# Kernel optimization log

Measured on AMD Instinct MI355X. Metric: run time of the kernel, lower is better.

## Reference

```python
import jax, jax.numpy as jnp
import numpy as np

FS, R, ULAW = 160, 2, 256  # frame_size, n_samples_per_step, 2**ulaw


def _conv1d(x, w, b):
    # x: [B,C,L], w: [O,I,3], VALID conv (PyTorch Conv1d, no padding)
    y = jax.lax.conv_general_dilated(x, w, (1,), 'VALID',
                                     dimension_numbers=('NCH', 'OIH', 'NCH'))
    return y + b[None, :, None]


def _gru(x, Wih, Whh, bih, bhh):
    # PyTorch GRU (batch_first), gate order r,z,n. x: [B,T,In] -> [B,T,H]
    B = x.shape[0]
    H = Whh.shape[1]
    xW = jnp.einsum('bti,gi->btg', x, Wih) + bih  # precompute input gates [B,T,3H]
    def step(h, xw):
        gh = h @ Whh.T + bhh
        r = jax.nn.sigmoid(xw[:, :H] + gh[:, :H])
        z = jax.nn.sigmoid(xw[:, H:2 * H] + gh[:, H:2 * H])
        n = jnp.tanh(xw[:, 2 * H:] + r * gh[:, 2 * H:])
        h = (1.0 - z) * n + z * h
        return h, h
    h0 = jnp.zeros((B, H), x.dtype)
    _, ys = jax.lax.scan(step, h0, jnp.swapaxes(xW, 0, 1))
    return jnp.swapaxes(ys, 0, 1)


def _mdense(x, w1, w2, b1, b2, f1, f2):
    return jnp.tanh(x @ w1.T + b1) * f1 + jnp.tanh(x @ w2.T + b2) * f2


def setup_inputs() -> dict:
    key = jax.random.key(0)
    ks = jax.random.split(key, 40)
    B, NF, NBF = 64, 15, 20
    T = (NF - 4) * FS  # 1760: two VALID k=3 convs -> 11 frames
    EP, ES, DF, H1, H2 = 64, 128, 128, 384, 16
    IN_A = 3 * ES * R + DF   # 896
    IN_B = H1 + DF           # 512
    p = lambda k, shape, s=0.1: (s * jax.random.normal(k, shape)).astype(jnp.float32)
    d = {
        'in_data': jax.random.randint(ks[0], (B, T, 3), 0, ULAW),
        'features': jax.random.normal(ks[1], (B, NF, NBF), jnp.float32),
        'periods': jax.random.randint(ks[2], (B, NF, 1), 0, 256),
        'targets': jax.random.randint(ks[3], (B, T), 0, ULAW),
        'embed_pitch': p(ks[4], (256, EP)),
        'embed_sig': p(ks[5], (ULAW, ES)),
        'conv1_w': p(ks[6], (DF, EP + NBF, 3)), 'conv1_b': p(ks[7], (DF,)),
        'conv2_w': p(ks[8], (DF, DF, 3)), 'conv2_b': p(ks[9], (DF,)),
        'fd1_w': p(ks[10], (DF, DF)), 'fd1_b': p(ks[11], (DF,)),
        'fd2_w': p(ks[12], (DF, DF)), 'fd2_b': p(ks[13], (DF,)),
        'ga_wih': p(ks[14], (3 * H1, IN_A)), 'ga_whh': p(ks[15], (3 * H1, H1)),
        'ga_bih': p(ks[16], (3 * H1,)), 'ga_bhh': p(ks[17], (3 * H1,)),
        'gb_wih': p(ks[18], (3 * H2, IN_B)), 'gb_whh': p(ks[19], (3 * H2, H2)),
        'gb_bih': p(ks[20], (3 * H2,)), 'gb_bhh': p(ks[21], (3 * H2,)),
        'md1_w1': p(ks[22], (ULAW, H2)), 'md1_w2': p(ks[23], (ULAW, H2)),
        'md1_b1': p(ks[24], (ULAW,)), 'md1_b2': p(ks[25], (ULAW,)),
        'md1_f1': jnp.ones((ULAW,), jnp.float32), 'md1_f2': jnp.ones((ULAW,), jnp.float32),
        'md2_w1': p(ks[26], (ULAW, H2 + ES)), 'md2_w2': p(ks[27], (ULAW, H2 + ES)),
        'md2_b1': p(ks[28], (ULAW,)), 'md2_b2': p(ks[29], (ULAW,)),
        'md2_f1': jnp.ones((ULAW,), jnp.float32), 'md2_f2': jnp.ones((ULAW,), jnp.float32),
    }
    return d


def reference(in_data, features, periods, targets, embed_pitch, embed_sig,
              conv1_w, conv1_b, conv2_w, conv2_b, fd1_w, fd1_b, fd2_w, fd2_b,
              ga_wih, ga_whh, ga_bih, ga_bhh, gb_wih, gb_whh, gb_bih, gb_bhh,
              md1_w1, md1_w2, md1_b1, md1_b2, md1_f1, md1_f2,
              md2_w1, md2_w2, md2_b1, md2_b2, md2_f1, md2_f2):
    B, T = targets.shape
    # frame-rate feature network
    pitch = embed_pitch[periods[..., 0]]                  # [B,15,EP]
    cat = jnp.concatenate([features, pitch], axis=-1)      # [B,15,NBF+EP]
    x = jnp.swapaxes(cat, 1, 2)                            # [B,C,15]
    x = jnp.tanh(_conv1d(x, conv1_w, conv1_b))
    x = jnp.tanh(_conv1d(x, conv2_w, conv2_b))             # [B,DF,11]
    f = jnp.swapaxes(x, 1, 2)
    f = jnp.tanh(f @ fd1_w.T + fd1_b)
    f = jnp.tanh(f @ fd2_w.T + fd2_b)                      # [B,11,DF]
    rep = jnp.repeat(f, FS // R, axis=1)                   # [B,880,DF]
    # sample-rate network (bunched: R samples per step)
    emb = embed_sig[in_data].reshape(B, T, -1).reshape(B, T // R, -1)  # [B,880,3*ES*R]
    rnn_in = jnp.concatenate([emb, rep], axis=-1)
    g1 = _gru(rnn_in, ga_wih, ga_whh, ga_bih, ga_bhh)      # [B,880,H1]
    g2 = _gru(jnp.concatenate([g1, rep], axis=-1), gb_wih, gb_whh, gb_bih, gb_bhh)  # [B,880,H2]
    o1 = _mdense(g2, md1_w1, md1_w2, md1_b1, md1_b2, md1_f1, md1_f2)  # [B,880,ULAW]
    # teacher forcing (p_teacher_forcing = 1.0): even-index targets feed branch 2
    pred_exc = targets[:, 0::R]                            # [B,880]
    ctx = jnp.concatenate([g2, embed_sig[pred_exc]], axis=-1)
    o2 = _mdense(ctx, md2_w1, md2_w2, md2_b1, md2_b2, md2_f1, md2_f2)
    # strided scatter: out[:, ::2]=o1, out[:, 1::2]=o2 == interleave
    out = jnp.stack([o1, o2], axis=2).reshape(B, T, ULAW)
    return out
```

## Files before the change

### kernel.cpp

```cpp
#include <hip/hip_runtime.h>
#include <hip/hip_bf16.h>
#include <hip/hip_fp16.h>

#define NF    15
#define NBF   20
#define TT    1760
#define TS    880
#define EP    64
#define ES    128
#define DF    128
#define H1    384
#define G3    1152
#define INA   896
#define JREP  11

typedef _Float16 h2v __attribute__((ext_vector_type(2)));

__device__ __forceinline__ float sigmf_(float x){ return 1.0f/(1.0f + __expf(-x)); }
__device__ __forceinline__ float tanhf_(float x){ return 2.0f/(1.0f + __expf(-2.0f*x)) - 1.0f; }
__device__ __forceinline__ h2v bc_h2(unsigned u){ return __builtin_bit_cast(h2v, u); }
__device__ __forceinline__ float fdot2_(h2v a, h2v b, float c){
#if __has_builtin(__builtin_amdgcn_fdot2)
  return __builtin_amdgcn_fdot2(a, b, c, false);
#else
  return c + (float)a[0]*(float)b[0] + (float)a[1]*(float)b[1];
#endif
}
__device__ __forceinline__ unsigned pk2_(float a, float b){
#if __has_builtin(__builtin_amdgcn_cvt_pkrtz)
  return __builtin_bit_cast(unsigned, __builtin_amdgcn_cvt_pkrtz(a, b));
#else
  unsigned lo = (unsigned)__builtin_bit_cast(unsigned short, (_Float16)a);
  unsigned hi = (unsigned)__builtin_bit_cast(unsigned short, (_Float16)b);
  return lo | (hi << 16);
#endif
}
__device__ __forceinline__ void bar_lgkm(){
  asm volatile("s_waitcnt lgkmcnt(0)" ::: "memory");
  __builtin_amdgcn_s_barrier();
  __builtin_amdgcn_sched_barrier(0);
}

__global__ __launch_bounds__(128) void k_frame(const float* feat, const int* periods, const float* embp,
   const float* c1w, const float* c1b, const float* c2w, const float* c2b,
   const float* f1w, const float* f1b, const float* f2w, const float* f2b, float* fout)
{
  __shared__ float cat[NF*84];
  __shared__ float x1[13*DF];
  __shared__ float x2[JREP*DF];
  int b = blockIdx.x, tid = threadIdx.x;
  for (int idx = tid; idx < NF*84; idx += 128){
    int j = idx/84, c = idx%84;
    cat[idx] = (c < NBF) ? feat[(b*NF+j)*NBF + c]
                         : embp[periods[b*NF+j]*EP + (c-NBF)];
  }
  __syncthreads();
  int o = tid;
  for (int p = 0; p < 13; ++p){
    float acc = c1b[o];
    for (int kk = 0; kk < 3; ++kk)
      for (int c = 0; c < 84; ++c)
        acc += cat[(p+kk)*84 + c] * c1w[(o*84+c)*3+kk];
    x1[p*DF+o] = tanhf_(acc);
  }
  __syncthreads();
  for (int p = 0; p < JREP; ++p){
    float acc = c2b[o];
    for (int kk = 0; kk < 3; ++kk)
      for (int c = 0; c < DF; ++c)
        acc += x1[(p+kk)*DF+c] * c2w[(o*DF+c)*3+kk];
    x2[p*DF+o] = tanhf_(acc);
  }
  __syncthreads();
  for (int p = 0; p < JREP; ++p){
    float acc = f1b[o];
    for (int c = 0; c < DF; ++c) acc += x2[p*DF+c]*f1w[o*DF+c];
    x1[p*DF+o] = tanhf_(acc);
  }
  __syncthreads();
  for (int p = 0; p < JREP; ++p){
    float acc = f2b[o];
    for (int c = 0; c < DF; ++c) acc += x1[p*DF+c]*f2w[o*DF+c];
    fout[(b*JREP+p)*DF+o] = tanhf_(acc);
  }
}

__global__ __launch_bounds__(256) void k_wpack5(const float* whh, _Float16* wpk){
  int o = blockIdx.x*256 + threadIdx.x;
  int hu = o & 1;
  int c  = (o >> 1) & 3;
  int idx = o >> 3;
  int tid = idx % 768;
  int n   = (idx / 768) % 18;
  int hf  = idx / (768*18);
  int i = tid % 384, u = tid / 384;
  int gd = n*4 + c;
  int m = gd / 12, dc = gd % 12;
  int pos  = (dc % 2) + 2*(dc / 6);
  int gate = (dc % 6) >> 1;
  int j = hf*96 + u*48 + (4*m + pos)*2 + hu;
  wpk[o] = (_Float16)whh[(gate*H1 + i)*H1 + j];
}

__global__ __launch_bounds__(256) void k_tables(const float* wih, const float* emb, float* GA){
  __shared__ float Wl[64*129];
  int k = blockIdx.x/18, g0 = (blockIdx.x%18)*64;
  int tid = threadIdx.x;
  for (int idx = tid; idx < 64*128; idx += 256){
    int gg = idx>>7, c = idx&127;
    Wl[gg*129+c] = wih[(size_t)(g0+gg)*INA + k*128 + c];
  }
  __syncthreads();
  int vv = tid>>6, gg = tid&63;
  for (int v = vv; v < 256; v += 4){
    const float* e = emb + (size_t)v*ES;
    float acc = 0.f;
    for (int c = 0; c < 128; ++c) acc += e[c]*Wl[gg*129+c];
    GA[(size_t)(k*256+v)*G3 + g0+gg] = acc;
  }
}

__global__ __launch_bounds__(256) void k_xwrepA(const float* wih, const float* f,
                                                const float* bih, const float* bhh, float* xwA){
  __shared__ float Wl[64*129];
  int g0 = blockIdx.x*64, tid = threadIdx.x;
  for (int idx = tid; idx < 64*128; idx += 256){
    int gg = idx>>7, c = idx&127;
    Wl[gg*129+c] = wih[(size_t)(g0+gg)*INA + 768 + c];
  }
  __syncthreads();
  int vv = tid>>6, gg = tid&63; int g = g0+gg;
  float badd = bih[g] + (g < 768 ? bhh[g] : 0.f);
  for (int row = vv; row < 64*JREP; row += 4){
    const float* fr = f + (size_t)row*DF;
    float acc = badd;
    for (int c = 0; c < 128; ++c) acc += fr[c]*Wl[gg*129+c];
    xwA[(size_t)row*G3 + g] = acc;
  }
}

__global__ __launch_bounds__(256) void k_xwrepB(const float* wih, const float* f,
                                                const float* bih, const float* bhh, float* xwB){
  __shared__ float Wl[48*129];
  int b = blockIdx.x, tid = threadIdx.x;
  for (int idx = tid; idx < 48*128; idx += 256){
    int r = idx>>7, c = idx&127;
    Wl[r*129+c] = wih[r*512 + 384 + c];
  }
  __syncthreads();
  for (int idx = tid; idx < JREP*48; idx += 256){
    int j = idx/48, r = idx%48;
    const float* fr = f + (size_t)(b*JREP+j)*DF;
    float acc = bih[r] + (r < 32 ? bhh[r] : 0.f);
    for (int c = 0; c < 128; ++c) acc += fr[c]*Wl[r*129+c];
    xwB[(size_t)(b*JREP+j)*48 + r] = acc;
  }
}

__global__ __launch_bounds__(256) void k_t2(const float* w1, const float* w2, const float* emb, float* T2){
  __shared__ float Wl[64*129];
  int tbl = blockIdx.x>>2; int c0 = (blockIdx.x&3)*64; int tid = threadIdx.x;
  const float* w = tbl ? w2 : w1;
  for (int idx = tid; idx < 64*128; idx += 256){
    int cc = idx>>7, e = idx&127;
    Wl[cc*129+e] = w[(c0+cc)*144 + 16 + e];
  }
  __syncthreads();
  int vv = tid>>6, cc = tid&63;
  for (int v = vv; v < 256; v += 4){
    const float* e = emb + (size_t)v*ES;
    float acc = 0.f;
    for (int c = 0; c < 128; ++c) acc += e[c]*Wl[cc*129+c];
    T2[tbl*65536 + v*256 + c0+cc] = acc;
  }
}

#define LD18(n) uint4 d##n = wsrc[(size_t)(n)*768];
#define Q2(A,B,C, q2) { \
  h2v hA = hh[jb2 + (q2)*2],     hB = hh[jb2 + (q2)*2 + 1]; \
  ar = fdot2_(hA, bc_h2(A.x), ar); ar = fdot2_(hB, bc_h2(A.y), ar); \
  az = fdot2_(hA, bc_h2(A.z), az); az = fdot2_(hB, bc_h2(A.w), az); \
  an = fdot2_(hA, bc_h2(B.x), an); an = fdot2_(hB, bc_h2(B.y), an); \
  h2v hC = hh[jb2 + (q2)*2 + 2], hD = hh[jb2 + (q2)*2 + 3]; \
  ar = fdot2_(hC, bc_h2(B.z), ar); ar = fdot2_(hD, bc_h2(B.w), ar); \
  az = fdot2_(hC, bc_h2(C.x), az); az = fdot2_(hD, bc_h2(C.y), az); \
  an = fdot2_(hC, bc_h2(C.z), an); an = fdot2_(hD, bc_h2(C.w), an); }
#define DOTS12 \
  Q2(d0,d1,d2,0) Q2(d3,d4,d5,2) Q2(d6,d7,d8,4) \
  Q2(d9,d10,d11,6) Q2(d12,d13,d14,8) Q2(d15,d16,d17,10)

#define PLW(n, p) { unsigned w = __hip_atomic_load((p), __ATOMIC_RELAXED, __HIP_MEMORY_SCOPE_AGENT); \
                    rv##n = w; ok &= ((w & 1023u) == tg); }

__global__ __launch_bounds__(768, 3) void k_scanA9(const int* __restrict__ in_data,
        const float* __restrict__ GA, const float* __restrict__ xwA,
        const uint4* __restrict__ wpk, const float* __restrict__ bhh,
        unsigned* __restrict__ g1u, unsigned* pbuf)
{
  __shared__ __align__(16) unsigned h16u[48];
  __shared__ __align__(8)  float pg[3][2][384];
  __shared__ __align__(8)  float xwb[2][G3];
  __shared__ int indr[2][8];
  const int P = blockIdx.x;
  const int b = P & 63, hf = P >> 6;
  const int tid = threadIdx.x;
  const int i  = tid % 384;
  const int u  = tid / 384;
  const int jb2 = u * 24;
  const int* ind_b = in_data + (size_t)b*TT*3;

  const uint4* wsrc = wpk + (size_t)(hf*18)*768 + tid;
  LD18(0) LD18(1) LD18(2) LD18(3) LD18(4) LD18(5) LD18(6) LD18(7) LD18(8)
  LD18(9) LD18(10) LD18(11) LD18(12) LD18(13) LD18(14) LD18(15) LD18(16) LD18(17)

  const bool isGat = (tid < 576);
  const int  c0 = 2*tid, c1 = 2*tid + 1;
  const bool isPub = (tid >= 96 && tid < 672);
  const int  po0 = 2*(tid - 96);

  float hreg0 = 0.f, hreg1 = 0.f, bn0 = 0.f, bn1 = 0.f;
  if (tid < 48){
    bn0 = bhh[768 + hf*96 + 2*tid];
    bn1 = bhh[768 + hf*96 + 2*tid + 1];
    h16u[tid] = 0u;
  }
  if (isGat){
    float s0 = xwA[(size_t)(b*JREP)*G3 + c0];
    float s1 = xwA[(size_t)(b*JREP)*G3 + c1];
    #pragma unroll
    for (int k2 = 0; k2 < 6; ++k2){
      int v = ind_b[k2];
      s0 += GA[((size_t)k2*256 + v)*G3 + c0];
      s1 += GA[((size_t)k2*256 + v)*G3 + c1];
    }
    xwb[0][c0] = s0; xwb[0][c1] = s1;
  }
  if (tid >= 576 && tid < 582) indr[1][tid-576] = ind_b[6 + (tid-576)];

  unsigned* pbo = pbuf + ((size_t)(b*4 + hf)*2)*G3;
  const int pf1 = (hf+1)&3, pf2 = (hf+2)&3, pf3 = (hf+3)&3;
  const unsigned* pb1 = pbuf + ((size_t)(b*4 + pf1)*2)*G3 + hf*96 + 2*(tid<48?tid:0);
  const unsigned* pb2 = pbuf + ((size_t)(b*4 + pf2)*2)*G3 + hf*96 + 2*(tid<48?tid:0);
  const unsigned* pb3 = pbuf + ((size_t)(b*4 + pf3)*2)*G3 + hf*96 + 2*(tid<48?tid:0);
  const h2v* hh = (const h2v*)h16u;
  __syncthreads();

  for (int t = 0; t < TS; ++t){
    const int nb = t & 1;
    const int tp = t + 1;
    float ga0=0.f,ga1=0.f,ga2=0.f,ga3=0.f,ga4=0.f,ga5=0.f,gx0=0.f;
    float gb0=0.f,gb1=0.f,gb2=0.f,gb3=0.f,gb4=0.f,gb5=0.f,gx1=0.f;
    if (tp < TS && isGat){
      int v0=indr[tp&1][0], v1=indr[tp&1][1], v2=indr[tp&1][2];
      int v3=indr[tp&1][3], v4=indr[tp&1][4], v5=indr[tp&1][5];
      const float* xwr = xwA + ((size_t)(b*JREP) + tp/80)*G3;
      ga0 = GA[((size_t)0*256 + v0)*G3 + c0]; gb0 = GA[((size_t)0*256 + v0)*G3 + c1];
      ga1 = GA[((size_t)1*256 + v1)*G3 + c0]; gb1 = GA[((size_t)1*256 + v1)*G3 + c1];
      ga2 = GA[((size_t)2*256 + v2)*G3 + c0]; gb2 = GA[((size_t)2*256 + v2)*G3 + c1];
      ga3 = GA[((size_t)3*256 + v3)*G3 + c0]; gb3 = GA[((size_t)3*256 + v3)*G3 + c1];
      ga4 = GA[((size_t)4*256 + v4)*G3 + c0]; gb4 = GA[((size_t)4*256 + v4)*G3 + c1];
      ga5 = GA[((size_t)5*256 + v5)*G3 + c0]; gb5 = GA[((size_t)5*256 + v5)*G3 + c1];
      gx0 = xwr[c0]; gx1 = xwr[c1];
    }
    int iv = 0;
    const int stg = t + 2;
    const bool doStg = (tid >= 576 && tid < 582 && stg < TS);
    if (doStg) iv = ind_b[6*stg + (tid-576)];
    float ar=0.f, az=0.f, an=0.f;
    DOTS12
    pg[0][u][i] = ar; pg[1][u][i] = az; pg[2][u][i] = an;
    if (tp < TS && isGat){
      xwb[tp&1][c0] = ga0+ga1+ga2+ga3+ga4+ga5+gx0;
      xwb[tp&1][c1] = gb0+gb1+gb2+gb3+gb4+gb5+gx1;
    }
    if (doStg) indr[t&1][tid-576] = iv;
    bar_lgkm();
    if (isPub){
      int g = po0/384, ii = po0 - g*384;
      float2 p0 = *(const float2*)&pg[g][0][ii];
      float2 p1 = *(const float2*)&pg[g][1][ii];
      float v0 = p0.x + p1.x, v1 = p0.y + p1.y;
      unsigned tw0 = (__builtin_bit_cast(unsigned, v0) & 0xFFFFFC00u) | (unsigned)t;
      unsigned tw1 = (__builtin_bit_cast(unsigned, v1) & 0xFFFFFC00u) | (unsigned)t;
      unsigned* dst = pbo + (size_t)nb*G3 + po0;
      __hip_atomic_store(dst,     tw0, __ATOMIC_RELAXED, __HIP_MEMORY_SCOPE_AGENT);
      __hip_atomic_store(dst + 1, tw1, __ATOMIC_RELAXED, __HIP_MEMORY_SCOPE_AGENT);
    } else if (tid < 48){
      const unsigned tg = (unsigned)t;
      const unsigned* q1 = pb1 + (size_t)nb*G3;
      const unsigned* q2 = pb2 + (size_t)nb*G3;
      const unsigned* q3 = pb3 + (size_t)nb*G3;
      unsigned rv0,rv1,rv2,rv3,rv4,rv5,rv6,rv7,rv8;
      unsigned rv9,rv10,rv11,rv12,rv13,rv14,rv15,rv16,rv17;
      bool ok;
      do {
        ok = true;
        PLW(0,  q1+0) PLW(1,  q1+1) PLW(2,  q1+384) PLW(3,  q1+385) PLW(4,  q1+768) PLW(5,  q1+769)
        PLW(6,  q2+0) PLW(7,  q2+1) PLW(8,  q2+384) PLW(9,  q2+385) PLW(10, q2+768) PLW(11, q2+769)
        PLW(12, q3+0) PLW(13, q3+1) PLW(14, q3+384) PLW(15, q3+385) PLW(16, q3+768) PLW(17, q3+769)
        if (!ok) __builtin_amdgcn_s_sleep(1);
      } while (!ok);
      __builtin_amdgcn_sched_barrier(0);
      #define FV(n) __builtin_bit_cast(float, rv##n & 0xFFFFFC00u)
      int i0 = hf*96 + 2*tid;
      float2 o0 = *(const float2*)&pg[0][0][i0];  float2 o0b = *(const float2*)&pg[0][1][i0];
      float2 o1 = *(const float2*)&pg[1][0][i0];  float2 o1b = *(const float2*)&pg[1][1][i0];
      float2 o2 = *(const float2*)&pg[2][0][i0];  float2 o2b = *(const float2*)&pg[2][1][i0];
      float2 xr = *(const float2*)&xwb[nb][i0];
      float2 xz = *(const float2*)&xwb[nb][384 + i0];
      float2 xn = *(const float2*)&xwb[nb][768 + i0];
      float R0 = o0.x + o0b.x + FV(0)  + FV(6)  + FV(12) + xr.x;
      float R1 = o0.y + o0b.y + FV(1)  + FV(7)  + FV(13) + xr.y;
      float Z0 = o1.x + o1b.x + FV(2)  + FV(8)  + FV(14) + xz.x;
      float Z1 = o1.y + o1b.y + FV(3)  + FV(9)  + FV(15) + xz.y;
      float G0 = o2.x + o2b.x + FV(4)  + FV(10) + FV(16) + bn0;
      float G1 = o2.y + o2b.y + FV(5)  + FV(11) + FV(17) + bn1;
      #undef FV
      float rr0 = sigmf_(R0), zz0 = sigmf_(Z0);
      float nn0 = tanhf_(xn.x + rr0*G0);
      float h0 = (1.f - zz0)*nn0 + zz0*hreg0; hreg0 = h0;
      float rr1 = sigmf_(R1), zz1 = sigmf_(Z1);
      float nn1 = tanhf_(xn.y + rr1*G1);
      float h1 = (1.f - zz1)*nn1 + zz1*hreg1; hreg1 = h1;
      unsigned pack = pk2_(h0, h1);
      h16u[tid] = pack;
      g1u[((size_t)b*TS + t)*192 + hf*48 + tid] = pack;
    }
    bar_lgkm();
  }
}

__global__ __launch_bounds__(256) void k_xwB(const _Float16* g1, const float* wih,
                                             const float* xwrB, float* xwB){
  __shared__ _Float16 gl[16*392];
  int bi = blockIdx.x; int b = bi/55; int t0 = (bi%55)*16; int tid = threadIdx.x;
  for (int idx = tid; idx < 16*H1; idx += 256){
    int tt = idx/H1, c = idx%H1;
    gl[tt*392+c] = g1[((size_t)b*TS + t0+tt)*H1 + c];
  }
  __syncthreads();
  int rr = tid>>4, tt = tid&15;
  int t = t0+tt;
  const float* xr = xwrB + ((size_t)(b*JREP) + t/80)*48;
  for (int rb = 0; rb < 3; ++rb){
    int r = rb*16 + rr;
    const float* wrow = wih + (size_t)r*512;
    float acc = 0.f;
    for (int c = 0; c < H1; ++c) acc += (float)gl[tt*392+c]*wrow[c];
    xwB[((size_t)b*TS + t)*48 + r] = acc + xr[r];
  }
}

__global__ __launch_bounds__(64) void k_scanB(const float* xwB, const float* whh,
                                              const float* bhh, float* g2){
  __shared__ float wl[48*17];
  __shared__ float h2s[16];
  __shared__ float pre[32];
  __shared__ float xn[16], gn[16];
  int b = blockIdx.x, tid = threadIdx.x;
  for (int idx = tid; idx < 768; idx += 64) wl[(idx>>4)*17 + (idx&15)] = whh[idx];
  if (tid < 16) h2s[tid] = 0.f;
  float bn = (tid >= 32 && tid < 48) ? bhh[tid] : 0.f;
  __syncthreads();
  for (int t = 0; t < TS; ++t){
    if (tid < 48){
      float xw = xwB[((size_t)b*TS + t)*48 + tid];
      float gh = 0.f;
      for (int e = 0; e < 16; ++e) gh += wl[tid*17+e]*h2s[e];
      if (tid < 32) pre[tid] = xw + gh;
      else { xn[tid-32] = xw; gn[tid-32] = gh + bn; }
    }
    __syncthreads();
    if (tid < 16){
      float r = sigmf_(pre[tid]), z = sigmf_(pre[16+tid]);
      float n = tanhf_(xn[tid] + r*gn[tid]);
      float hn = (1.f - z)*n + z*h2s[tid];
      h2s[tid] = hn;
      g2[((size_t)b*TS + t)*16 + tid] = hn;
    }
    __syncthreads();
  }
}

__global__ __launch_bounds__(256) void k_out(const float* g2, const int* targets, const float* T2,
    const float* m1w1, const float* m1w2, const float* m1b1, const float* m1b2,
    const float* m1f1, const float* m1f2,
    const float* m2w1, const float* m2w2, const float* m2b1, const float* m2b2,
    const float* m2f1, const float* m2f2, float* out)
{
  __shared__ float wA[256*17], wB[256*17], wC[256*17], wD[256*17];
  __shared__ float g2l[16*16];
  int bi = blockIdx.x; int b = bi/55; int t0 = (bi%55)*16; int c = threadIdx.x;
  for (int d = 0; d < 16; ++d){
    wA[c*17+d] = m1w1[c*16+d];  wB[c*17+d] = m1w2[c*16+d];
    wC[c*17+d] = m2w1[c*144+d]; wD[c*17+d] = m2w2[c*144+d];
  }
  { int tt = c>>4, d = c&15; g2l[c] = g2[((size_t)b*TS + t0+tt)*16 + d]; }
  __syncthreads();
  float b1a = m1b1[c], b2a = m1b2[c], f1a = m1f1[c], f2a = m1f2[c];
  float b1b = m2b1[c], b2b = m2b2[c], f1b = m2f1[c], f2b = m2f2[c];
  for (int tt = 0; tt < 16; ++tt){
    int t = t0+tt;
    float d1 = b1a, d2 = b2a, e1 = b1b, e2 = b2b;
    for (int d = 0; d < 16; ++d){
      float g = g2l[tt*16+d];
      d1 += g*wA[c*17+d]; d2 += g*wB[c*17+d];
      e1 += g*wC[c*17+d]; e2 += g*wD[c*17+d];
    }
    int v = targets[b*TT + 2*t];
    e1 += T2[v*256+c]; e2 += T2[65536 + v*256+c];
    float o1 = f1a*tanhf_(d1) + f2a*tanhf_(d2);
    float o2 = f1b*tanhf_(e1) + f2b*tanhf_(e2);
    size_t base = ((size_t)b*TS + t)*2*256;
    out[base + c]       = o1;
    out[base + 256 + c] = o2;
  }
}

extern "C" void kernel_launch(void* const* d_in, const int* in_sizes, int n_in,
                              void* d_out, int out_size, void* d_ws, size_t ws_size,
                              hipStream_t stream) {
  const int*   in_data = (const int*)  d_in[0];
  const float* feat    = (const float*)d_in[1];
  const int*   periods = (const int*)  d_in[2];
  const int*   targets = (const int*)  d_in[3];
  const float* embp    = (const float*)d_in[4];
  const float* embs    = (const float*)d_in[5];
  const float* c1w = (const float*)d_in[6];  const float* c1b = (const float*)d_in[7];
  const float* c2w = (const float*)d_in[8];  const float* c2b = (const float*)d_in[9];
  const float* f1w = (const float*)d_in[10]; const float* f1b = (const float*)d_in[11];
  const float* f2w = (const float*)d_in[12]; const float* f2b = (const float*)d_in[13];
  const float* ga_wih = (const float*)d_in[14]; const float* ga_whh = (const float*)d_in[15];
  const float* ga_bih = (const float*)d_in[16]; const float* ga_bhh = (const float*)d_in[17];
  const float* gb_wih = (const float*)d_in[18]; const float* gb_whh = (const float*)d_in[19];
  const float* gb_bih = (const float*)d_in[20]; const float* gb_bhh = (const float*)d_in[21];
  const float* m1w1 = (const float*)d_in[22]; const float* m1w2 = (const float*)d_in[23];
  const float* m1b1 = (const float*)d_in[24]; const float* m1b2 = (const float*)d_in[25];
  const float* m1f1 = (const float*)d_in[26]; const float* m1f2 = (const float*)d_in[27];
  const float* m2w1 = (const float*)d_in[28]; const float* m2w2 = (const float*)d_in[29];
  const float* m2b1 = (const float*)d_in[30]; const float* m2b2 = (const float*)d_in[31];
  const float* m2f1 = (const float*)d_in[32]; const float* m2f2 = (const float*)d_in[33];
  float* out = (float*)d_out;

  float* GA     = (float*)d_ws;
  float* xWrepA = GA     + 1769472;
  float* xWrepB = xWrepA + 811008;
  float* fbuf   = xWrepB + 33792;
  float* xWB    = fbuf   + 90112;
  float* g2buf  = xWB    + 2703360;
  float* T2     = g2buf  + 901120;
  _Float16* Wpk = (_Float16*)(T2 + 131072);
  unsigned* pbuf = (unsigned*)(Wpk + 442368);
  _Float16* g1  = (_Float16*)d_out;

  (void)hipMemsetAsync(pbuf, 0xFF, 589824*sizeof(unsigned), stream);
  hipLaunchKernelGGL(k_frame, dim3(64), dim3(128), 0, stream,
                     feat, periods, embp, c1w, c1b, c2w, c2b, f1w, f1b, f2w, f2b, fbuf);
  hipLaunchKernelGGL(k_wpack5, dim3(1728), dim3(256), 0, stream, ga_whh, Wpk);
  hipLaunchKernelGGL(k_tables, dim3(108), dim3(256), 0, stream, ga_wih, embs, GA);
  hipLaunchKernelGGL(k_t2, dim3(8), dim3(256), 0, stream, m2w1, m2w2, embs, T2);
  hipLaunchKernelGGL(k_xwrepA, dim3(18), dim3(256), 0, stream, ga_wih, fbuf, ga_bih, ga_bhh, xWrepA);
  hipLaunchKernelGGL(k_xwrepB, dim3(64), dim3(256), 0, stream, gb_wih, fbuf, gb_bih, gb_bhh, xWrepB);
  hipLaunchKernelGGL(k_scanA9, dim3(256), dim3(768), 0, stream,
                     in_data, GA, xWrepA, (const uint4*)Wpk, ga_bhh,
                     (unsigned*)g1, pbuf);
  hipLaunchKernelGGL(k_xwB, dim3(64*55), dim3(256), 0, stream, g1, gb_wih, xWrepB, xWB);
  hipLaunchKernelGGL(k_scanB, dim3(64), dim3(64), 0, stream, xWB, gb_whh, gb_bhh, g2buf);
  hipLaunchKernelGGL(k_out, dim3(64*55), dim3(256), 0, stream,
                     g2buf, targets, T2, m1w1, m1w2, m1b1, m1b2, m1f1, m1f2,
                     m2w1, m2w2, m2b1, m2b2, m2f1, m2f2, out);
}
```

Before: 4.094 ms.

## Batch four sequences per GRU-A scan block and pack k_xwB weights to fp16

```diff
diff --git a/kernel.cpp b/kernel.cpp
--- a/kernel.cpp
+++ b/kernel.cpp
@@ -192,22 +192,62 @@
 #define PLW(n, p) { unsigned w = __hip_atomic_load((p), __ATOMIC_RELAXED, __HIP_MEMORY_SCOPE_AGENT); \
                     rv##n = w; ok &= ((w & 1023u) == tg); }
 
-__global__ __launch_bounds__(768, 3) void k_scanA9(const int* __restrict__ in_data,
+#define PHASE(m) { \
+  const int tp = t + 1; \
+  float ga0=0.f,ga1=0.f,ga2=0.f,ga3=0.f,ga4=0.f,ga5=0.f,gx0=0.f; \
+  float gb0=0.f,gb1=0.f,gb2=0.f,gb3=0.f,gb4=0.f,gb5=0.f,gx1=0.f; \
+  if (tp < TS && isGat){ \
+    int v0=indr[m][tp&1][0], v1=indr[m][tp&1][1], v2=indr[m][tp&1][2]; \
+    int v3=indr[m][tp&1][3], v4=indr[m][tp&1][4], v5=indr[m][tp&1][5]; \
+    const float* xwr = xwA + ((size_t)((gq*4+m)*JREP) + tp/80)*G3; \
+    ga0 = GA[((size_t)0*256 + v0)*G3 + c0]; gb0 = GA[((size_t)0*256 + v0)*G3 + c1]; \
+    ga1 = GA[((size_t)1*256 + v1)*G3 + c0]; gb1 = GA[((size_t)1*256 + v1)*G3 + c1]; \
+    ga2 = GA[((size_t)2*256 + v2)*G3 + c0]; gb2 = GA[((size_t)2*256 + v2)*G3 + c1]; \
+    ga3 = GA[((size_t)3*256 + v3)*G3 + c0]; gb3 = GA[((size_t)3*256 + v3)*G3 + c1]; \
+    ga4 = GA[((size_t)4*256 + v4)*G3 + c0]; gb4 = GA[((size_t)4*256 + v4)*G3 + c1]; \
+    ga5 = GA[((size_t)5*256 + v5)*G3 + c0]; gb5 = GA[((size_t)5*256 + v5)*G3 + c1]; \
+    gx0 = xwr[c0]; gx1 = xwr[c1]; \
+  } \
+  int iv = 0; \
+  if ((m) == 0 && doStg && (t+2) < TS) \
+    iv = in_data[(size_t)(gq*4+stgM)*TT*3 + 6*(t+2) + stgK]; \
+  float ar=0.f, az=0.f, an=0.f; \
+  { const h2v* hh = (const h2v*)&h16u[m][0]; DOTS12 } \
+  pg[m][0][u][i] = ar; pg[m][1][u][i] = az; pg[m][2][u][i] = an; \
+  if (tp < TS && isGat){ \
+    xwb[m][tp&1][c0] = ga0+ga1+ga2+ga3+ga4+ga5+gx0; \
+    xwb[m][tp&1][c1] = gb0+gb1+gb2+gb3+gb4+gb5+gx1; \
+  } \
+  if ((m) == 0 && doStg && (t+2) < TS) indr[stgM][t&1][stgK] = iv; \
+  bar_lgkm(); \
+  if (isPub){ \
+    int po0 = 2*(tid - 192); int gg = po0/384, ii = po0 - gg*384; \
+    float2 p0 = *(const float2*)&pg[m][gg][0][ii]; \
+    float2 p1 = *(const float2*)&pg[m][gg][1][ii]; \
+    float v0f = p0.x + p1.x, v1f = p0.y + p1.y; \
+    unsigned tw0 = (__builtin_bit_cast(unsigned, v0f) & 0xFFFFFC00u) | (unsigned)(t & 1023); \
+    unsigned tw1 = (__builtin_bit_cast(unsigned, v1f) & 0xFFFFFC00u) | (unsigned)(t & 1023); \
+    unsigned* dst = pbuf + ((size_t)((gq*4+m)*4 + hf)*2 + nb)*G3 + po0; \
+    __hip_atomic_store(dst,   tw0, __ATOMIC_RELAXED, __HIP_MEMORY_SCOPE_AGENT); \
+    __hip_atomic_store(dst+1, tw1, __ATOMIC_RELAXED, __HIP_MEMORY_SCOPE_AGENT); \
+  } \
+}
+
+__global__ __launch_bounds__(768, 3) void k_scanA12(const int* __restrict__ in_data,
         const float* __restrict__ GA, const float* __restrict__ xwA,
         const uint4* __restrict__ wpk, const float* __restrict__ bhh,
         unsigned* __restrict__ g1u, unsigned* pbuf)
 {
-  __shared__ __align__(16) unsigned h16u[48];
-  __shared__ __align__(8)  float pg[3][2][384];
-  __shared__ __align__(8)  float xwb[2][G3];
-  __shared__ int indr[2][8];
+  __shared__ __align__(16) unsigned h16u[4][48];
+  __shared__ __align__(8)  float pg[4][3][2][384];
+  __shared__ __align__(8)  float xwb[4][2][G3];
+  __shared__ int indr[4][2][8];
   const int P = blockIdx.x;
-  const int b = P & 63, hf = P >> 6;
+  const int gq = P >> 2, hf = P & 3;
   const int tid = threadIdx.x;
   const int i  = tid % 384;
   const int u  = tid / 384;
   const int jb2 = u * 24;
-  const int* ind_b = in_data + (size_t)b*TT*3;
 
   const uint4* wsrc = wpk + (size_t)(hf*18)*768 + tid;
   LD18(0) LD18(1) LD18(2) LD18(3) LD18(4) LD18(5) LD18(6) LD18(7) LD18(8)
@@ -215,81 +255,64 @@
 
   const bool isGat = (tid < 576);
   const int  c0 = 2*tid, c1 = 2*tid + 1;
-  const bool isPub = (tid >= 96 && tid < 672);
-  const int  po0 = 2*(tid - 96);
-
+  const bool isPub = (tid >= 192);
+  const bool doStg = (tid >= 576 && tid < 600);
+  const int  stgM = doStg ? (tid-576)/6 : 0;
+  const int  stgK = doStg ? (tid-576)%6 : 0;
+
+  const int meW = tid >> 6;
+  const int l   = tid & 63;
+  const bool isEpi = (meW < 4) && (l < 48);
   float hreg0 = 0.f, hreg1 = 0.f, bn0 = 0.f, bn1 = 0.f;
-  if (tid < 48){
-    bn0 = bhh[768 + hf*96 + 2*tid];
-    bn1 = bhh[768 + hf*96 + 2*tid + 1];
-    h16u[tid] = 0u;
-  }
+  size_t g1base = 0;
+  const unsigned *eq1 = pbuf, *eq2 = pbuf, *eq3 = pbuf;
+  if (isEpi){
+    bn0 = bhh[768 + hf*96 + 2*l];
+    bn1 = bhh[768 + hf*96 + 2*l + 1];
+    int bb = gq*4 + meW;
+    g1base = (size_t)bb*TS*192 + hf*48 + l;
+    eq1 = pbuf + ((size_t)(bb*4 + ((hf+1)&3))*2)*G3 + hf*96 + 2*l;
+    eq2 = pbuf + ((size_t)(bb*4 + ((hf+2)&3))*2)*G3 + hf*96 + 2*l;
+    eq3 = pbuf + ((size_t)(bb*4 + ((hf+3)&3))*2)*G3 + hf*96 + 2*l;
+  }
+  if (tid < 192) ((unsigned*)h16u)[tid] = 0u;
+
   if (isGat){
-    float s0 = xwA[(size_t)(b*JREP)*G3 + c0];
-    float s1 = xwA[(size_t)(b*JREP)*G3 + c1];
     #pragma unroll
-    for (int k2 = 0; k2 < 6; ++k2){
-      int v = ind_b[k2];
-      s0 += GA[((size_t)k2*256 + v)*G3 + c0];
-      s1 += GA[((size_t)k2*256 + v)*G3 + c1];
+    for (int m = 0; m < 4; ++m){
+      const int* ib = in_data + (size_t)(gq*4+m)*TT*3;
+      float s0 = xwA[(size_t)((gq*4+m)*JREP)*G3 + c0];
+      float s1 = xwA[(size_t)((gq*4+m)*JREP)*G3 + c1];
+      #pragma unroll
+      for (int k2 = 0; k2 < 6; ++k2){
+        int v = ib[k2];
+        s0 += GA[((size_t)k2*256 + v)*G3 + c0];
+        s1 += GA[((size_t)k2*256 + v)*G3 + c1];
+      }
+      xwb[m][0][c0] = s0; xwb[m][0][c1] = s1;
     }
-    xwb[0][c0] = s0; xwb[0][c1] = s1;
-  }
-  if (tid >= 576 && tid < 582) indr[1][tid-576] = ind_b[6 + (tid-576)];
-
-  unsigned* pbo = pbuf + ((size_t)(b*4 + hf)*2)*G3;
-  const int pf1 = (hf+1)&3, pf2 = (hf+2)&3, pf3 = (hf+3)&3;
-  const unsigned* pb1 = pbuf + ((size_t)(b*4 + pf1)*2)*G3 + hf*96 + 2*(tid<48?tid:0);
-  const unsigned* pb2 = pbuf + ((size_t)(b*4 + pf2)*2)*G3 + hf*96 + 2*(tid<48?tid:0);
-  const unsigned* pb3 = pbuf + ((size_t)(b*4 + pf3)*2)*G3 + hf*96 + 2*(tid<48?tid:0);
-  const h2v* hh = (const h2v*)h16u;
+  }
+  if (doStg) indr[stgM][1][stgK] = in_data[(size_t)(gq*4+stgM)*TT*3 + 6 + stgK];
   __syncthreads();
 
   for (int t = 0; t < TS; ++t){
     const int nb = t & 1;
-    const int tp = t + 1;
-    float ga0=0.f,ga1=0.f,ga2=0.f,ga3=0.f,ga4=0.f,ga5=0.f,gx0=0.f;
-    float gb0=0.f,gb1=0.f,gb2=0.f,gb3=0.f,gb4=0.f,gb5=0.f,gx1=0.f;
-    if (tp < TS && isGat){
-      int v0=indr[tp&1][0], v1=indr[tp&1][1], v2=indr[tp&1][2];
-      int v3=indr[tp&1][3], v4=indr[tp&1][4], v5=indr[tp&1][5];
-      const float* xwr = xwA + ((size_t)(b*JREP) + tp/80)*G3;
-      ga0 = GA[((size_t)0*256 + v0)*G3 + c0]; gb0 = GA[((size_t)0*256 + v0)*G3 + c1];
-      ga1 = GA[((size_t)1*256 + v1)*G3 + c0]; gb1 = GA[((size_t)1*256 + v1)*G3 + c1];
-      ga2 = GA[((size_t)2*256 + v2)*G3 + c0]; gb2 = GA[((size_t)2*256 + v2)*G3 + c1];
-      ga3 = GA[((size_t)3*256 + v3)*G3 + c0]; gb3 = GA[((size_t)3*256 + v3)*G3 + c1];
-      ga4 = GA[((size_t)4*256 + v4)*G3 + c0]; gb4 = GA[((size_t)4*256 + v4)*G3 + c1];
-      ga5 = GA[((size_t)5*256 + v5)*G3 + c0]; gb5 = GA[((size_t)5*256 + v5)*G3 + c1];
-      gx0 = xwr[c0]; gx1 = xwr[c1];
-    }
-    int iv = 0;
-    const int stg = t + 2;
-    const bool doStg = (tid >= 576 && tid < 582 && stg < TS);
-    if (doStg) iv = ind_b[6*stg + (tid-576)];
-    float ar=0.f, az=0.f, an=0.f;
-    DOTS12
-    pg[0][u][i] = ar; pg[1][u][i] = az; pg[2][u][i] = an;
-    if (tp < TS && isGat){
-      xwb[tp&1][c0] = ga0+ga1+ga2+ga3+ga4+ga5+gx0;
-      xwb[tp&1][c1] = gb0+gb1+gb2+gb3+gb4+gb5+gx1;
-    }
-    if (doStg) indr[t&1][tid-576] = iv;
-    bar_lgkm();
-    if (isPub){
-      int g = po0/384, ii = po0 - g*384;
-      float2 p0 = *(const float2*)&pg[g][0][ii];
-      float2 p1 = *(const float2*)&pg[g][1][ii];
-      float v0 = p0.x + p1.x, v1 = p0.y + p1.y;
-      unsigned tw0 = (__builtin_bit_cast(unsigned, v0) & 0xFFFFFC00u) | (unsigned)t;
-      unsigned tw1 = (__builtin_bit_cast(unsigned, v1) & 0xFFFFFC00u) | (unsigned)t;
-      unsigned* dst = pbo + (size_t)nb*G3 + po0;
-      __hip_atomic_store(dst,     tw0, __ATOMIC_RELAXED, __HIP_MEMORY_SCOPE_AGENT);
-      __hip_atomic_store(dst + 1, tw1, __ATOMIC_RELAXED, __HIP_MEMORY_SCOPE_AGENT);
-    } else if (tid < 48){
-      const unsigned tg = (unsigned)t;
-      const unsigned* q1 = pb1 + (size_t)nb*G3;
-      const unsigned* q2 = pb2 + (size_t)nb*G3;
-      const unsigned* q3 = pb3 + (size_t)nb*G3;
+    PHASE(0)
+    PHASE(1)
+    PHASE(2)
+    PHASE(3)
+    if (isEpi){
+      int i0 = hf*96 + 2*l;
+      float2 o0 = *(const float2*)&pg[meW][0][0][i0];  float2 o0b = *(const float2*)&pg[meW][0][1][i0];
+      float2 o1 = *(const float2*)&pg[meW][1][0][i0];  float2 o1b = *(const float2*)&pg[meW][1][1][i0];
+      float2 o2 = *(const float2*)&pg[meW][2][0][i0];  float2 o2b = *(const float2*)&pg[meW][2][1][i0];
+      float2 xr = *(const float2*)&xwb[meW][nb][i0];
+      float2 xz = *(const float2*)&xwb[meW][nb][384 + i0];
+      float2 xn = *(const float2*)&xwb[meW][nb][768 + i0];
+      const unsigned tg = (unsigned)t & 1023u;
+      const unsigned* q1 = eq1 + (size_t)nb*G3;
+      const unsigned* q2 = eq2 + (size_t)nb*G3;
+      const unsigned* q3 = eq3 + (size_t)nb*G3;
       unsigned rv0,rv1,rv2,rv3,rv4,rv5,rv6,rv7,rv8;
       unsigned rv9,rv10,rv11,rv12,rv13,rv14,rv15,rv16,rv17;
       bool ok;
@@ -301,21 +324,14 @@
         if (!ok) __builtin_amdgcn_s_sleep(1);
       } while (!ok);
       __builtin_amdgcn_sched_barrier(0);
-      #define FV(n) __builtin_bit_cast(float, rv##n & 0xFFFFFC00u)
-      int i0 = hf*96 + 2*tid;
-      float2 o0 = *(const float2*)&pg[0][0][i0];  float2 o0b = *(const float2*)&pg[0][1][i0];
-      float2 o1 = *(const float2*)&pg[1][0][i0];  float2 o1b = *(const float2*)&pg[1][1][i0];
-      float2 o2 = *(const float2*)&pg[2][0][i0];  float2 o2b = *(const float2*)&pg[2][1][i0];
-      float2 xr = *(const float2*)&xwb[nb][i0];
-      float2 xz = *(const float2*)&xwb[nb][384 + i0];
-      float2 xn = *(const float2*)&xwb[nb][768 + i0];
-      float R0 = o0.x + o0b.x + FV(0)  + FV(6)  + FV(12) + xr.x;
-      float R1 = o0.y + o0b.y + FV(1)  + FV(7)  + FV(13) + xr.y;
-      float Z0 = o1.x + o1b.x + FV(2)  + FV(8)  + FV(14) + xz.x;
-      float Z1 = o1.y + o1b.y + FV(3)  + FV(9)  + FV(15) + xz.y;
-      float G0 = o2.x + o2b.x + FV(4)  + FV(10) + FV(16) + bn0;
-      float G1 = o2.y + o2b.y + FV(5)  + FV(11) + FV(17) + bn1;
-      #undef FV
+      #define FVV(n) __builtin_bit_cast(float, rv##n & 0xFFFFFC00u)
+      float R0 = o0.x + o0b.x + FVV(0)  + FVV(6)  + FVV(12) + xr.x;
+      float R1 = o0.y + o0b.y + FVV(1)  + FVV(7)  + FVV(13) + xr.y;
+      float Z0 = o1.x + o1b.x + FVV(2)  + FVV(8)  + FVV(14) + xz.x;
+      float Z1 = o1.y + o1b.y + FVV(3)  + FVV(9)  + FVV(15) + xz.y;
+      float G0 = o2.x + o2b.x + FVV(4)  + FVV(10) + FVV(16) + bn0;
+      float G1 = o2.y + o2b.y + FVV(5)  + FVV(11) + FVV(17) + bn1;
+      #undef FVV
       float rr0 = sigmf_(R0), zz0 = sigmf_(Z0);
       float nn0 = tanhf_(xn.x + rr0*G0);
       float h0 = (1.f - zz0)*nn0 + zz0*hreg0; hreg0 = h0;
@@ -323,30 +339,37 @@
       float nn1 = tanhf_(xn.y + rr1*G1);
       float h1 = (1.f - zz1)*nn1 + zz1*hreg1; hreg1 = h1;
       unsigned pack = pk2_(h0, h1);
-      h16u[tid] = pack;
-      g1u[((size_t)b*TS + t)*192 + hf*48 + tid] = pack;
+      h16u[meW][l] = pack;
+      g1u[g1base + (size_t)t*192] = pack;
     }
     bar_lgkm();
   }
 }
 
-__global__ __launch_bounds__(256) void k_xwB(const _Float16* g1, const float* wih,
+__global__ __launch_bounds__(256) void k_xwB(const unsigned* g1u, const float* wih,
                                              const float* xwrB, float* xwB){
-  __shared__ _Float16 gl[16*392];
+  __shared__ __align__(16) unsigned gl[16*194];
+  __shared__ __align__(16) unsigned wl[48*194];
   int bi = blockIdx.x; int b = bi/55; int t0 = (bi%55)*16; int tid = threadIdx.x;
-  for (int idx = tid; idx < 16*H1; idx += 256){
-    int tt = idx/H1, c = idx%H1;
-    gl[tt*392+c] = g1[((size_t)b*TS + t0+tt)*H1 + c];
+  for (int idx = tid; idx < 48*192; idx += 256){
+    int r = idx/192, cp = idx%192;
+    wl[r*194+cp] = pk2_(wih[r*512 + 2*cp], wih[r*512 + 2*cp + 1]);
+  }
+  for (int idx = tid; idx < 16*192; idx += 256){
+    int tt = idx/192, c = idx%192;
+    gl[tt*194+c] = g1u[((size_t)b*TS + t0+tt)*192 + c];
   }
   __syncthreads();
   int rr = tid>>4, tt = tid&15;
   int t = t0+tt;
   const float* xr = xwrB + ((size_t)(b*JREP) + t/80)*48;
+  const h2v* gp = (const h2v*)&gl[tt*194];
   for (int rb = 0; rb < 3; ++rb){
     int r = rb*16 + rr;
-    const float* wrow = wih + (size_t)r*512;
+    const h2v* wp_ = (const h2v*)&wl[r*194];
     float acc = 0.f;
-    for (int c = 0; c < H1; ++c) acc += (float)gl[tt*392+c]*wrow[c];
+    #pragma unroll 8
+    for (int c = 0; c < 192; ++c) acc = fdot2_(gp[c], wp_[c], acc);
     xwB[((size_t)b*TS + t)*48 + r] = acc + xr[r];
   }
 }
@@ -361,11 +384,14 @@
   for (int idx = tid; idx < 768; idx += 64) wl[(idx>>4)*17 + (idx&15)] = whh[idx];
   if (tid < 16) h2s[tid] = 0.f;
   float bn = (tid >= 32 && tid < 48) ? bhh[tid] : 0.f;
+  float xw_n = (tid < 48) ? xwB[(size_t)b*TS*48 + tid] : 0.f;
   __syncthreads();
   for (int t = 0; t < TS; ++t){
+    float xw = xw_n;
+    if (t+1 < TS && tid < 48) xw_n = xwB[((size_t)b*TS + t+1)*48 + tid];
     if (tid < 48){
-      float xw = xwB[((size_t)b*TS + t)*48 + tid];
       float gh = 0.f;
+      #pragma unroll
       for (int e = 0; e < 16; ++e) gh += wl[tid*17+e]*h2s[e];
       if (tid < 32) pre[tid] = xw + gh;
       else { xn[tid-32] = xw; gn[tid-32] = gh + bn; }
@@ -461,10 +487,11 @@
   hipLaunchKernelGGL(k_t2, dim3(8), dim3(256), 0, stream, m2w1, m2w2, embs, T2);
   hipLaunchKernelGGL(k_xwrepA, dim3(18), dim3(256), 0, stream, ga_wih, fbuf, ga_bih, ga_bhh, xWrepA);
   hipLaunchKernelGGL(k_xwrepB, dim3(64), dim3(256), 0, stream, gb_wih, fbuf, gb_bih, gb_bhh, xWrepB);
-  hipLaunchKernelGGL(k_scanA9, dim3(256), dim3(768), 0, stream,
+  hipLaunchKernelGGL(k_scanA12, dim3(64), dim3(768), 0, stream,
                      in_data, GA, xWrepA, (const uint4*)Wpk, ga_bhh,
                      (unsigned*)g1, pbuf);
-  hipLaunchKernelGGL(k_xwB, dim3(64*55), dim3(256), 0, stream, g1, gb_wih, xWrepB, xWB);
+  hipLaunchKernelGGL(k_xwB, dim3(64*55), dim3(256), 0, stream,
+                     (const unsigned*)g1, gb_wih, xWrepB, xWB);
   hipLaunchKernelGGL(k_scanB, dim3(64), dim3(64), 0, stream, xWB, gb_whh, gb_bhh, g2buf);
   hipLaunchKernelGGL(k_out, dim3(64*55), dim3(256), 0, stream,
                      g2buf, targets, T2, m1w1, m1w2, m1b1, m1b2, m1f1, m1f2,
```

Measured after the change: 9.369 ms. 2.29x slower.
